# Kernel optimization log

Measured on AMD Instinct MI355X. Metric: run time of the kernel, lower is better.

The kernel has to match this reference:

```python
import jax, jax.numpy as jnp
import numpy as np

NB_NEIGHBORS = 8
RADIUS = 0.5
SPLIT = 32
FEATURE_SIZE = 128
OUTPUT_SIZE = 64
MIDDLE = (FEATURE_SIZE + OUTPUT_SIZE) // 2  # 96
N = 100000


def setup_inputs() -> dict:
    key = jax.random.key(0)
    ks = jax.random.split(key, 8)
    points = jax.random.normal(ks[0], (N, 3), dtype=jnp.float32)
    features = jax.random.normal(ks[1], (N, SPLIT + FEATURE_SIZE), dtype=jnp.float32)
    batch = jnp.sort(jax.random.randint(ks[2], (N,), 0, 16)).astype(jnp.int64)
    # neighborhood decoder modeled as Linear(split -> nb_neighbors*3)
    dec_W = jax.random.normal(ks[3], (SPLIT, NB_NEIGHBORS * 3), dtype=jnp.float32) / np.sqrt(SPLIT)
    dec_b = jnp.zeros((NB_NEIGHBORS * 3,), dtype=jnp.float32)
    fc1_W = jax.random.normal(ks[4], (FEATURE_SIZE + 3, MIDDLE), dtype=jnp.float32) / np.sqrt(FEATURE_SIZE + 3)
    fc1_b = jnp.zeros((MIDDLE,), dtype=jnp.float32)
    fc2_W = jax.random.normal(ks[5], (MIDDLE, OUTPUT_SIZE), dtype=jnp.float32) / np.sqrt(MIDDLE)
    fc2_b = jnp.zeros((OUTPUT_SIZE,), dtype=jnp.float32)
    return {"points": points, "features": features, "batch": batch,
            "dec_W": dec_W, "dec_b": dec_b,
            "fc1_W": fc1_W, "fc1_b": fc1_b,
            "fc2_W": fc2_W, "fc2_b": fc2_b}


def reference(points, features, batch, dec_W, dec_b, fc1_W, fc1_b, fc2_W, fc2_b):
    # split incoming features
    point_features = features[:, :SPLIT]            # [N, split] -> neighborhood decoder
    feature_features = features[:, SPLIT:]          # [N, feature_size]
    # neighborhood decoder: nb_neighbors relative 3-D points per input point
    relative_points = (point_features @ dec_W + dec_b).reshape(-1, 3)   # [N*nb, 3]
    output_batch = jnp.repeat(batch, NB_NEIGHBORS, axis=0)              # [N*nb]
    # gather features to each generated neighbor, concat with relative coords
    features_repeated = jnp.repeat(feature_features, NB_NEIGHBORS, axis=0)  # [N*nb, feature_size]
    concat_features = jnp.concatenate([relative_points, features_repeated], axis=1)  # [N*nb, 3+feature_size]
    # 2-layer MLP with ReLU
    fc1_features = jax.nn.relu(concat_features @ fc1_W + fc1_b)
    fc2_features = jax.nn.relu(fc1_features @ fc2_W + fc2_b)
    # scaled residual add onto anchor points
    anchor_points = jnp.repeat(points, NB_NEIGHBORS, axis=0)  # [N*nb, 3]
    output_points = anchor_points + relative_points * RADIUS
    return (output_points, fc2_features, output_batch)
```

## Files before the change

kernel.cpp:

```cpp
#include <hip/hip_runtime.h>
#include <hip/hip_bf16.h>

typedef __bf16 bf16x8 __attribute__((ext_vector_type(8)));
typedef float  f32x4  __attribute__((ext_vector_type(4)));

__device__ __forceinline__ ushort f2b(float f){
  union { float f; uint i; } v; v.f = f; uint u = v.i;
  return (ushort)((u + 0x7FFFu + ((u >> 16) & 1u)) >> 16);
}
__device__ __forceinline__ uint pack2(float a, float b){
  __hip_bfloat162 h = __float22bfloat162_rn(make_float2(a, b));
  union { __hip_bfloat162 h; uint u; } v; v.h = h; return v.u;
}
__device__ __forceinline__ bf16x8 ldfrag(const ushort* p){
  return *reinterpret_cast<const bf16x8*>(p);
}
__device__ __forceinline__ f32x4 relu4(f32x4 x){
  f32x4 r;
  r[0]=fmaxf(x[0],0.f); r[1]=fmaxf(x[1],0.f);
  r[2]=fmaxf(x[2],0.f); r[3]=fmaxf(x[3],0.f);
  return r;
}

__global__ void omd_transpose(const float* __restrict__ fc1W, const float* __restrict__ fc2W,
                              const float* __restrict__ decW,
                              ushort* __restrict__ W1ftr, ushort* __restrict__ W2tr,
                              ushort* __restrict__ decWtr){
  int t = blockIdx.x * 256 + threadIdx.x;
  if (t < 96*128){
    int n = t >> 7, k = t & 127;
    W1ftr[t] = f2b(fc1W[(3 + k)*96 + n]);
  } else if (t < 96*128 + 64*96){
    int e = t - 96*128;
    int n = e / 96, k = e - n*96;
    W2tr[e] = f2b(fc2W[k*64 + n]);
  } else if (t < 96*128 + 64*96 + 32*32){
    int e = t - (96*128 + 64*96);
    int n = e >> 5, k = e & 31;
    decWtr[e] = (n < 24) ? f2b(decW[k*24 + n]) : (ushort)0;
  }
}

__global__ __launch_bounds__(256, 3) void omd_main(
    const float* __restrict__ points, const float* __restrict__ feats,
    const int*   __restrict__ batch,  const float* __restrict__ decb,
    const float* __restrict__ fc1W,   const float* __restrict__ fc1b,
    const float* __restrict__ fc2b,   const ushort* __restrict__ W1ftr,
    const ushort* __restrict__ W2tr,  const ushort* __restrict__ decWtr,
    float* __restrict__ out, int npts)
{
  __shared__ __align__(16) ushort pfB[32*40];
  __shared__ float decbL[24];
  __shared__ float w1pL[3*96];
  __shared__ float relL[32*24];
  __shared__ __align__(16) ushort ffL[32*136];
  __shared__ __align__(16) float  s1L[32*100];
  __shared__ __align__(16) ushort hL[2*32*104];

  const int t    = threadIdx.x;
  const int w    = t >> 6;
  const int lane = t & 63;
  const int q    = lane >> 4;
  const int c    = lane & 15;
  const int pbase = blockIdx.x * 32;

  const size_t offF = (size_t)npts * 24;
  const size_t offB = (size_t)npts * 24 + (size_t)npts * 512;

  {
    int p = t >> 3, seg = t & 7;
    const f32x4* src = (const f32x4*)(feats + (size_t)(pbase + p)*160);
    f32x4 f = src[seg];
    uint* dst = (uint*)pfB;
    dst[p*20 + seg*2    ] = pack2(f[0], f[1]);
    dst[p*20 + seg*2 + 1] = pack2(f[2], f[3]);
  }
  {
    int m = t >> 3, seg = t & 7;
    const f32x4* src = (const f32x4*)(feats + (size_t)(pbase + m)*160 + 32 + seg*16);
    uint* dst = (uint*)(ffL + m*136 + seg*16);
    #pragma unroll
    for (int r = 0; r < 4; ++r){
      f32x4 f = src[r];
      dst[r*2    ] = pack2(f[0], f[1]);
      dst[r*2 + 1] = pack2(f[2], f[3]);
    }
  }
  if (t < 24) decbL[t] = decb[t];
  for (int e = t; e < 288; e += 256) w1pL[e] = fc1W[e];

  bf16x8 w2f[4][3];
  #pragma unroll
  for (int nt = 0; nt < 4; ++nt)
    #pragma unroll
    for (int kt = 0; kt < 3; ++kt)
      w2f[nt][kt] = ldfrag(W2tr + (nt*16 + c)*96 + kt*32 + q*8);

  __syncthreads();

  {
    int mt = w & 1, ntile = w >> 1;
    bf16x8 a = ldfrag(pfB + (mt*16 + c)*40 + q*8);
    bf16x8 b = ldfrag(decWtr + ((ntile*16 + c)<<5) + q*8);
    f32x4 acc = {0.f, 0.f, 0.f, 0.f};
    acc = __builtin_amdgcn_mfma_f32_16x16x32_bf16(a, b, acc, 0, 0, 0);
    int n = ntile*16 + c;
    if (n < 24){
      float bb = decbL[n];
      #pragma unroll
      for (int r = 0; r < 4; ++r)
        relL[(mt*16 + q*4 + r)*24 + n] = acc[r] + bb;
    }
  }

  {
    int mt = w & 1, trio = w >> 1;
    const ushort* arow = ffL + (mt*16 + c)*136 + q*8;
    bf16x8 a0 = ldfrag(arow);
    bf16x8 a1 = ldfrag(arow + 32);
    bf16x8 a2 = ldfrag(arow + 64);
    bf16x8 a3 = ldfrag(arow + 96);
    #pragma unroll
    for (int i = 0; i < 3; ++i){
      const ushort* brow = W1ftr + ((trio*3 + i)*16 + c)*128 + q*8;
      f32x4 acc = {0.f, 0.f, 0.f, 0.f};
      acc = __builtin_amdgcn_mfma_f32_16x16x32_bf16(a0, ldfrag(brow      ), acc, 0, 0, 0);
      acc = __builtin_amdgcn_mfma_f32_16x16x32_bf16(a1, ldfrag(brow + 32 ), acc, 0, 0, 0);
      acc = __builtin_amdgcn_mfma_f32_16x16x32_bf16(a2, ldfrag(brow + 64 ), acc, 0, 0, 0);
      acc = __builtin_amdgcn_mfma_f32_16x16x32_bf16(a3, ldfrag(brow + 96 ), acc, 0, 0, 0);
      int col = (trio*3 + i)*16 + c;
      float bb = fc1b[col];
      #pragma unroll
      for (int r = 0; r < 4; ++r)
        s1L[(mt*16 + q*4 + r)*100 + col] = acc[r] + bb;
    }
  }
  __syncthreads();

  const int m  = t >> 3;
  const int jb = (t & 7) * 12;
  f32x4 s0, s1_, s2, wa0, wa1, wa2, wb0, wb1, wb2, wc0, wc1, wc2;
  {
    const f32x4* s1v = (const f32x4*)&s1L[m*100 + jb];
    s0 = s1v[0]; s1_ = s1v[1]; s2 = s1v[2];
    wa0 = *(const f32x4*)&w1pL[jb];     wa1 = *(const f32x4*)&w1pL[jb+4];     wa2 = *(const f32x4*)&w1pL[jb+8];
    wb0 = *(const f32x4*)&w1pL[96+jb];  wb1 = *(const f32x4*)&w1pL[96+jb+4];  wb2 = *(const f32x4*)&w1pL[96+jb+8];
    wc0 = *(const f32x4*)&w1pL[192+jb]; wc1 = *(const f32x4*)&w1pL[192+jb+4]; wc2 = *(const f32x4*)&w1pL[192+jb+8];
  }

  #pragma unroll 1
  for (int pair = 0; pair < 4; ++pair){
    {
      uint* hLu = (uint*)hL;
      #pragma unroll
      for (int nl = 0; nl < 2; ++nl){
        int n = pair*2 + nl;
        float r0 = relL[m*24 + 3*n], r1 = relL[m*24 + 3*n + 1], r2 = relL[m*24 + 3*n + 2];
        f32x4 h0 = relu4(s0  + r0*wa0 + r1*wb0 + r2*wc0);
        f32x4 h1 = relu4(s1_ + r0*wa1 + r1*wb1 + r2*wc1);
        f32x4 h2 = relu4(s2  + r0*wa2 + r1*wb2 + r2*wc2);
        int ub = nl*1664 + m*52 + (t & 7)*6;
        hLu[ub    ] = pack2(h0[0], h0[1]);
        hLu[ub + 1] = pack2(h0[2], h0[3]);
        hLu[ub + 2] = pack2(h1[0], h1[1]);
        hLu[ub + 3] = pack2(h1[2], h1[3]);
        hLu[ub + 4] = pack2(h2[0], h2[1]);
        hLu[ub + 5] = pack2(h2[2], h2[3]);
      }
    }
    __syncthreads();

    {
      int nl = w & 1, mtw = w >> 1;
      const ushort* hrow = hL + nl*3328 + (mtw*16 + c)*104 + q*8;
      bf16x8 ha0 = ldfrag(hrow);
      bf16x8 ha1 = ldfrag(hrow + 32);
      bf16x8 ha2 = ldfrag(hrow + 64);
      int n = pair*2 + nl;
      int prow0 = pbase + mtw*16 + q*4;
      #pragma unroll
      for (int nt = 0; nt < 4; ++nt){
        float bb = fc2b[nt*16 + c];
        f32x4 acc = {bb, bb, bb, bb};
        acc = __builtin_amdgcn_mfma_f32_16x16x32_bf16(ha0, w2f[nt][0], acc, 0, 0, 0);
        acc = __builtin_amdgcn_mfma_f32_16x16x32_bf16(ha1, w2f[nt][1], acc, 0, 0, 0);
        acc = __builtin_amdgcn_mfma_f32_16x16x32_bf16(ha2, w2f[nt][2], acc, 0, 0, 0);
        #pragma unroll
        for (int r = 0; r < 4; ++r){
          size_t g = (size_t)(prow0 + r)*8 + n;
          out[offF + g*64 + nt*16 + c] = fmaxf(acc[r], 0.f);
        }
      }
    }
    __syncthreads();
  }

  #pragma unroll
  for (int i = 0; i < 3; ++i){
    int e = t + 256*i;
    int p = e / 24, rem = e - p*24;
    int d = rem % 3;
    float v = points[(size_t)(pbase + p)*3 + d] + 0.5f * relL[e];
    out[(size_t)(pbase + p)*24 + rem] = v;
  }
  {
    int p = t >> 3, n = t & 7;
    out[offB + (size_t)(pbase + p)*8 + n] = (float)batch[pbase + p];
  }
}

extern "C" void kernel_launch(void* const* d_in, const int* in_sizes, int n_in,
                              void* d_out, int out_size, void* d_ws, size_t ws_size,
                              hipStream_t stream){
  const float* points = (const float*)d_in[0];
  const float* feats  = (const float*)d_in[1];
  const int*   batch  = (const int*)d_in[2];
  const float* decW   = (const float*)d_in[3];
  const float* decb   = (const float*)d_in[4];
  const float* fc1W   = (const float*)d_in[5];
  const float* fc1b   = (const float*)d_in[6];
  const float* fc2W   = (const float*)d_in[7];
  const float* fc2b   = (const float*)d_in[8];
  float*  outp   = (float*)d_out;
  ushort* W1ftr  = (ushort*)d_ws;
  ushort* W2tr   = W1ftr + 96*128;
  ushort* decWtr = W2tr + 64*96;

  int npts = in_sizes[2];

  omd_transpose<<<76, 256, 0, stream>>>(fc1W, fc2W, decW, W1ftr, W2tr, decWtr);
  omd_main<<<npts/32, 256, 0, stream>>>(points, feats, batch, decb,
                                        fc1W, fc1b, fc2b, W1ftr, W2tr, decWtr,
                                        outp, npts);
}
```

Before: 307.2 us.

## Build fc2 A-fragments in registers, removing LDS staging and per-pair barriers

The fc1 activation (s1 plus relative-point term, ReLU, bf16 pack) is now computed directly in the MFMA A-fragment layout in registers, so each wave feeds fc2 MFMAs without writing to and reading from an LDS buffer. This removes the hL shared buffer and the two __syncthreads per neighbor pair in the 4-iteration loop. Each wave now handles 4 neighbors for its 16-row tile, which requires 16 accumulator vectors and raises register pressure under launch_bounds(256,3). The freed LDS could also allow more resident blocks.

New measurement: 321.0 us. 1.04x slower.

```diff
diff --git a/kernel.cpp b/kernel.cpp
--- a/kernel.cpp
+++ b/kernel.cpp
@@ -51,11 +51,10 @@
 {
   __shared__ __align__(16) ushort pfB[32*40];
   __shared__ float decbL[24];
-  __shared__ float w1pL[3*96];
-  __shared__ float relL[32*24];
+  __shared__ __align__(16) float w1pL[3*96];
+  __shared__ __align__(16) float relL[32*24];
   __shared__ __align__(16) ushort ffL[32*136];
   __shared__ __align__(16) float  s1L[32*100];
-  __shared__ __align__(16) ushort hL[2*32*104];
 
   const int t    = threadIdx.x;
   const int w    = t >> 6;
@@ -137,62 +136,61 @@
   }
   __syncthreads();
 
-  const int m  = t >> 3;
-  const int jb = (t & 7) * 12;
-  f32x4 s0, s1_, s2, wa0, wa1, wa2, wb0, wb1, wb2, wc0, wc1, wc2;
-  {
-    const f32x4* s1v = (const f32x4*)&s1L[m*100 + jb];
-    s0 = s1v[0]; s1_ = s1v[1]; s2 = s1v[2];
-    wa0 = *(const f32x4*)&w1pL[jb];     wa1 = *(const f32x4*)&w1pL[jb+4];     wa2 = *(const f32x4*)&w1pL[jb+8];
-    wb0 = *(const f32x4*)&w1pL[96+jb];  wb1 = *(const f32x4*)&w1pL[96+jb+4];  wb2 = *(const f32x4*)&w1pL[96+jb+8];
-    wc0 = *(const f32x4*)&w1pL[192+jb]; wc1 = *(const f32x4*)&w1pL[192+jb+4]; wc2 = *(const f32x4*)&w1pL[192+jb+8];
-  }
-
-  #pragma unroll 1
-  for (int pair = 0; pair < 4; ++pair){
-    {
-      uint* hLu = (uint*)hL;
-      #pragma unroll
-      for (int nl = 0; nl < 2; ++nl){
-        int n = pair*2 + nl;
-        float r0 = relL[m*24 + 3*n], r1 = relL[m*24 + 3*n + 1], r2 = relL[m*24 + 3*n + 2];
-        f32x4 h0 = relu4(s0  + r0*wa0 + r1*wb0 + r2*wc0);
-        f32x4 h1 = relu4(s1_ + r0*wa1 + r1*wb1 + r2*wc1);
-        f32x4 h2 = relu4(s2  + r0*wa2 + r1*wb2 + r2*wc2);
-        int ub = nl*1664 + m*52 + (t & 7)*6;
-        hLu[ub    ] = pack2(h0[0], h0[1]);
-        hLu[ub + 1] = pack2(h0[2], h0[3]);
-        hLu[ub + 2] = pack2(h1[0], h1[1]);
-        hLu[ub + 3] = pack2(h1[2], h1[3]);
-        hLu[ub + 4] = pack2(h2[0], h2[1]);
-        hLu[ub + 5] = pack2(h2[2], h2[3]);
+  {
+    const int mt = w & 1, g = w >> 1;
+    const int row = mt*16 + c;
+
+    f32x4 ra = *(const f32x4*)&relL[row*24 + g*12];
+    f32x4 rb = *(const f32x4*)&relL[row*24 + g*12 + 4];
+    f32x4 rc = *(const f32x4*)&relL[row*24 + g*12 + 8];
+    float rl[4][3] = {{ra[0],ra[1],ra[2]},{ra[3],rb[0],rb[1]},
+                      {rb[2],rb[3],rc[0]},{rc[1],rc[2],rc[3]}};
+
+    f32x4 acc[4][4];
+    #pragma unroll
+    for (int nt = 0; nt < 4; ++nt){
+      float bb = fc2b[nt*16 + c];
+      #pragma unroll
+      for (int n = 0; n < 4; ++n) acc[n][nt] = (f32x4){bb, bb, bb, bb};
+    }
+
+    #pragma unroll
+    for (int kt = 0; kt < 3; ++kt){
+      const f32x4* s1v = (const f32x4*)&s1L[row*100 + kt*32 + q*8];
+      f32x4 sA = s1v[0], sB = s1v[1];
+      f32x4 wA0 = *(const f32x4*)&w1pL[      kt*32 + q*8];
+      f32x4 wB0 = *(const f32x4*)&w1pL[      kt*32 + q*8 + 4];
+      f32x4 wA1 = *(const f32x4*)&w1pL[ 96 + kt*32 + q*8];
+      f32x4 wB1 = *(const f32x4*)&w1pL[ 96 + kt*32 + q*8 + 4];
+      f32x4 wA2 = *(const f32x4*)&w1pL[192 + kt*32 + q*8];
+      f32x4 wB2 = *(const f32x4*)&w1pL[192 + kt*32 + q*8 + 4];
+      #pragma unroll
+      for (int n = 0; n < 4; ++n){
+        f32x4 hA = relu4(sA + rl[n][0]*wA0 + rl[n][1]*wA1 + rl[n][2]*wA2);
+        f32x4 hB = relu4(sB + rl[n][0]*wB0 + rl[n][1]*wB1 + rl[n][2]*wB2);
+        union { uint u[4]; bf16x8 v; } af;
+        af.u[0] = pack2(hA[0], hA[1]);
+        af.u[1] = pack2(hA[2], hA[3]);
+        af.u[2] = pack2(hB[0], hB[1]);
+        af.u[3] = pack2(hB[2], hB[3]);
+        #pragma unroll
+        for (int nt = 0; nt < 4; ++nt)
+          acc[n][nt] = __builtin_amdgcn_mfma_f32_16x16x32_bf16(af.v, w2f[nt][kt], acc[n][nt], 0, 0, 0);
       }
     }
-    __syncthreads();
-
-    {
-      int nl = w & 1, mtw = w >> 1;
-      const ushort* hrow = hL + nl*3328 + (mtw*16 + c)*104 + q*8;
-      bf16x8 ha0 = ldfrag(hrow);
-      bf16x8 ha1 = ldfrag(hrow + 32);
-      bf16x8 ha2 = ldfrag(hrow + 64);
-      int n = pair*2 + nl;
-      int prow0 = pbase + mtw*16 + q*4;
+
+    #pragma unroll
+    for (int n = 0; n < 4; ++n){
+      int nn = g*4 + n;
       #pragma unroll
       for (int nt = 0; nt < 4; ++nt){
-        float bb = fc2b[nt*16 + c];
-        f32x4 acc = {bb, bb, bb, bb};
-        acc = __builtin_amdgcn_mfma_f32_16x16x32_bf16(ha0, w2f[nt][0], acc, 0, 0, 0);
-        acc = __builtin_amdgcn_mfma_f32_16x16x32_bf16(ha1, w2f[nt][1], acc, 0, 0, 0);
-        acc = __builtin_amdgcn_mfma_f32_16x16x32_bf16(ha2, w2f[nt][2], acc, 0, 0, 0);
         #pragma unroll
         for (int r = 0; r < 4; ++r){
-          size_t g = (size_t)(prow0 + r)*8 + n;
-          out[offF + g*64 + nt*16 + c] = fmaxf(acc[r], 0.f);
+          size_t gg = (size_t)(pbase + mt*16 + q*4 + r)*8 + nn;
+          out[offF + gg*64 + nt*16 + c] = fmaxf(acc[n][nt][r], 0.f);
         }
       }
     }
-    __syncthreads();
   }
 
   #pragma unroll
```
